# Optimization experiments

Measured on AMD Instinct MI355X. Metric: run time of the kernel, lower is better.

The kernel has to match this reference:

```python
import jax, jax.numpy as jnp
import numpy as np

B, S, INPUT_DIM = 16, 2048, 768
G, V = 2, 320            # num_codebooks, codebook_size
D = INPUT_DIM // G       # codebook_dim = 384
OUT_DIM = 768
TEMP = 1.0
EPS = 1e-10


def setup_inputs() -> dict:
    key = jax.random.key(0)
    ks = jax.random.split(key, 7)
    z = jax.random.normal(ks[0], (B, S, INPUT_DIM), dtype=jnp.float32)
    noise = jax.random.uniform(ks[1], (B, S, G, V), dtype=jnp.float32)
    # logits_projection: Linear(codebook_dim -> codebook_size)
    W_logits = jax.random.normal(ks[2], (D, V), dtype=jnp.float32) / np.sqrt(D)
    b_logits = jnp.zeros((V,), dtype=jnp.float32)
    codebooks = jax.random.normal(ks[3], (G, V, D), dtype=jnp.float32)
    # output_projection: Linear(input_dim -> output_dim)
    W_out = jax.random.normal(ks[4], (INPUT_DIM, OUT_DIM), dtype=jnp.float32) / np.sqrt(INPUT_DIM)
    b_out = jnp.zeros((OUT_DIM,), dtype=jnp.float32)
    return {"z": z, "noise": noise, "W_logits": W_logits, "b_logits": b_logits,
            "codebooks": codebooks, "W_out": W_out, "b_out": b_out}


def reference(z, noise, W_logits, b_logits, codebooks, W_out, b_out):
    b, s, _ = z.shape
    g, v, d = codebooks.shape
    zr = z.reshape(b, s, g, d)                                   # [B,S,G,D]
    logits = jnp.einsum('bsgd,dv->bsgv', zr, W_logits) + b_logits
    # training-mode gumbel noise
    gumbel = -jnp.log(-jnp.log(noise + EPS) + EPS)
    logits = (logits + gumbel) / TEMP
    probs = jax.nn.softmax(logits, axis=-1)                      # [B,S,G,V]
    indices = jnp.argmax(probs, axis=-1)                         # [B,S,G]
    hard = jax.nn.one_hot(indices, v, dtype=probs.dtype)
    quantized = hard - jax.lax.stop_gradient(probs) + probs      # straight-through
    quantized = jnp.einsum('bsgv,gvd->bsgd', quantized, codebooks)
    quantized = quantized.reshape(b, s, g * d)
    return quantized @ W_out + b_out
```

## Files before the change

kernel.cpp:

```cpp
#include <hip/hip_runtime.h>
#include <math.h>

#define BS_TOT 32768
#define IN_DIM 768
#define G_N 2
#define V_N 320
#define D_N 384
#define OUT_N 768
#define EPS_F 1e-10f

typedef _Float16 f16x8 __attribute__((ext_vector_type(8)));
typedef float    f32x16 __attribute__((ext_vector_type(16)));

#define GLOBAL_LOAD_LDS16(gaddr, laddr)                                        \
  __builtin_amdgcn_global_load_lds(                                            \
      (const __attribute__((address_space(1))) unsigned int*)(gaddr),          \
      (__attribute__((address_space(3))) unsigned int*)(laddr), 16, 0, 0)

__global__ __launch_bounds__(256) void prep_w(
    const float* __restrict__ Wl, _Float16* __restrict__ Wp)
{
    int e = blockIdx.x * 256 + threadIdx.x;
    if (e >= D_N * V_N) return;
    int k = e / V_N, v = e - k * V_N;
    int kt = k >> 5, kl = k & 31, kh = kl >> 3, j = kl & 7;
    float w = Wl[e];
    _Float16 a = (_Float16)w;
    float r = (w - (float)a) * 4096.f;
    Wp[((size_t)((kt * 2 + 0) * 4 + kh) * V_N + v) * 8 + j] = a;
    Wp[((size_t)((kt * 2 + 1) * 4 + kh) * V_N + v) * 8 + j] = (_Float16)r;
}

__global__ __launch_bounds__(256) void precompute_P(
    const float* __restrict__ cb, const float* __restrict__ Wo,
    float* __restrict__ P)
{
    const int tid = threadIdx.x;
    const int c0  = blockIdx.x * 256;
    const int r0  = blockIdx.y * 8;
    const int g   = r0 / V_N;
    __shared__ float As[8][D_N];
    {
        const float4* src = (const float4*)(cb + (size_t)r0 * D_N);
        float4* dst = (float4*)(&As[0][0]);
        #pragma unroll
        for (int p = 0; p < 3; ++p) dst[tid + p * 256] = src[tid + p * 256];
    }
    __syncthreads();
    float acc[8];
    #pragma unroll
    for (int i = 0; i < 8; ++i) acc[i] = 0.f;
    const float* wp = Wo + ((size_t)g * D_N) * OUT_N + c0 + tid;
    for (int d = 0; d < D_N; d += 4) {
        float w0 = wp[(size_t)(d + 0) * OUT_N];
        float w1 = wp[(size_t)(d + 1) * OUT_N];
        float w2 = wp[(size_t)(d + 2) * OUT_N];
        float w3 = wp[(size_t)(d + 3) * OUT_N];
        #pragma unroll
        for (int i = 0; i < 8; ++i) {
            float4 a = *(const float4*)&As[i][d];
            acc[i] = fmaf(a.x, w0, acc[i]);
            acc[i] = fmaf(a.y, w1, acc[i]);
            acc[i] = fmaf(a.z, w2, acc[i]);
            acc[i] = fmaf(a.w, w3, acc[i]);
        }
    }
    #pragma unroll
    for (int i = 0; i < 8; ++i)
        P[(size_t)(r0 + i) * OUT_N + c0 + tid] = acc[i];
}

__global__ __launch_bounds__(256, 2) void logits_mfma(
    const float* __restrict__ z, const float* __restrict__ noise,
    const f16x8* __restrict__ Wp, const float* __restrict__ bl,
    int* __restrict__ idx)
{
    const int tid  = threadIdx.x;
    const int g    = blockIdx.y;
    const int m0   = blockIdx.x * 64;
    const int ln   = tid & 63;
    const int wv   = tid >> 6;
    const int wrow = wv >> 1;
    const int wcol = wv & 1;
    const int lh   = ln >> 5;
    const int l5   = ln & 31;

    __shared__ f16x8 BsV[2560];
    __shared__ f16x8 AsV[512];
    __shared__ float sVal[2][64];
    __shared__ int   sIdx[2][64];

    f32x16 accM[5], accC[5];
    #pragma unroll
    for (int nf = 0; nf < 5; ++nf)
        #pragma unroll
        for (int i = 0; i < 16; ++i) { accM[nf][i] = 0.f; accC[nf][i] = 0.f; }

    const int arow_s = tid & 63;
    const int akh    = tid >> 6;
    const float* zrow = z + (size_t)(m0 + arow_s) * IN_DIM + g * D_N + akh * 8;

    float4 ap0 = *(const float4*)(zrow);
    float4 ap1 = *(const float4*)(zrow + 4);

    const int arow = wrow * 32 + l5;
    const int bcol = wcol * 160 + l5;

    for (int kt = 0; kt < 12; ++kt) {
        __syncthreads();
        #pragma unroll
        for (int p = 0; p < 10; ++p) {
            GLOBAL_LOAD_LDS16(Wp + (size_t)kt * 2560 + wv * 640 + p * 64 + ln,
                              BsV + wv * 640 + p * 64);
        }
        {
            float x[8] = {ap0.x, ap0.y, ap0.z, ap0.w, ap1.x, ap1.y, ap1.z, ap1.w};
            f16x8 h1, h2;
            #pragma unroll
            for (int i = 0; i < 8; ++i) {
                _Float16 a = (_Float16)x[i];
                float r = (x[i] - (float)a) * 4096.f;
                h1[i] = a;
                h2[i] = (_Float16)r;
            }
            AsV[(0 * 4 + akh) * 64 + arow_s] = h1;
            AsV[(1 * 4 + akh) * 64 + arow_s] = h2;
        }
        __syncthreads();
        if (kt < 11) {
            ap0 = *(const float4*)(zrow + (kt + 1) * 32);
            ap1 = *(const float4*)(zrow + (kt + 1) * 32 + 4);
        }
        #pragma unroll
        for (int b = 0; b < 2; ++b) {
            f16x8 a0 = AsV[(0 * 4 + b * 2 + lh) * 64 + arow];
            f16x8 a1 = AsV[(1 * 4 + b * 2 + lh) * 64 + arow];
            #pragma unroll
            for (int nf = 0; nf < 5; ++nf) {
                f16x8 b0 = BsV[(0 * 4 + b * 2 + lh) * 320 + bcol + nf * 32];
                f16x8 b1 = BsV[(1 * 4 + b * 2 + lh) * 320 + bcol + nf * 32];
                accM[nf] = __builtin_amdgcn_mfma_f32_32x32x16_f16(a0, b0, accM[nf], 0, 0, 0);
                accC[nf] = __builtin_amdgcn_mfma_f32_32x32x16_f16(a0, b1, accC[nf], 0, 0, 0);
                accC[nf] = __builtin_amdgcn_mfma_f32_32x32x16_f16(a1, b0, accC[nf], 0, 0, 0);
            }
        }
    }

    float blv[5];
    #pragma unroll
    for (int nf = 0; nf < 5; ++nf) blv[nf] = bl[wcol * 160 + nf * 32 + l5];

    #pragma unroll
    for (int r = 0; r < 16; ++r) {
        const int rowloc = (r & 3) + 8 * (r >> 2) + 4 * lh;
        const int grow   = m0 + wrow * 32 + rowloc;
        const float* np_ = noise + ((size_t)grow * G_N + g) * V_N + wcol * 160 + l5;
        float best = -INFINITY; int bi = 0;
        #pragma unroll
        for (int nf = 0; nf < 5; ++nf) {
            float u   = np_[nf * 32];
            float gum = -__logf(-__logf(u + EPS_F) + EPS_F);
            float v   = accM[nf][r] + 2.44140625e-4f * accC[nf][r] + blv[nf] + gum;
            int   c   = wcol * 160 + nf * 32 + l5;
            if (v > best) { best = v; bi = c; }
        }
        #pragma unroll
        for (int off = 1; off < 32; off <<= 1) {
            float ov = __shfl_xor(best, off);
            int   oi = __shfl_xor(bi, off);
            if (ov > best || (ov == best && oi < bi)) { best = ov; bi = oi; }
        }
        if (l5 == 0) {
            sVal[wcol][wrow * 32 + rowloc] = best;
            sIdx[wcol][wrow * 32 + rowloc] = bi;
        }
    }
    __syncthreads();
    if (tid < 64) {
        float v0 = sVal[0][tid], v1 = sVal[1][tid];
        int   i0 = sIdx[0][tid], i1 = sIdx[1][tid];
        int   b  = (v1 > v0 || (v1 == v0 && i1 < i0)) ? i1 : i0;
        idx[(size_t)(m0 + tid) * G_N + g] = b;
    }
}

__global__ __launch_bounds__(256) void gather_out(
    const float* __restrict__ P, const int* __restrict__ idx,
    const float* __restrict__ bo, float* __restrict__ out)
{
    const int tid  = threadIdx.x;
    const int row0 = blockIdx.x << 2;
    #pragma unroll
    for (int p = 0; p < 3; ++p) {
        int f   = tid + (p << 8);
        int rl  = f / 192;
        int c4  = f - rl * 192;
        int row = row0 + rl;
        int i0  = idx[row * 2];
        int i1  = idx[row * 2 + 1];
        float4 a  = ((const float4*)(P + (size_t)i0 * OUT_N))[c4];
        float4 b2 = ((const float4*)(P + (size_t)(V_N + i1) * OUT_N))[c4];
        float4 c  = ((const float4*)bo)[c4];
        float4 r;
        r.x = a.x + b2.x + c.x;
        r.y = a.y + b2.y + c.y;
        r.z = a.z + b2.z + c.z;
        r.w = a.w + b2.w + c.w;
        ((float4*)(out + (size_t)row * OUT_N))[c4] = r;
    }
}

extern "C" void kernel_launch(void* const* d_in, const int* in_sizes, int n_in,
                              void* d_out, int out_size, void* d_ws, size_t ws_size,
                              hipStream_t stream)
{
    const float* z     = (const float*)d_in[0];
    const float* noise = (const float*)d_in[1];
    const float* Wl    = (const float*)d_in[2];
    const float* bl    = (const float*)d_in[3];
    const float* cb    = (const float*)d_in[4];
    const float* Wo    = (const float*)d_in[5];
    const float* bo    = (const float*)d_in[6];
    float* out = (float*)d_out;

    float*     P   = (float*)d_ws;
    int*       idx = (int*)((char*)d_ws + 1966080);
    _Float16*  Wp  = (_Float16*)((char*)d_ws + 2228224);

    prep_w<<<(D_N * V_N + 255) / 256, 256, 0, stream>>>(Wl, Wp);

    dim3 gA(OUT_N / 256, (G_N * V_N) / 8);
    precompute_P<<<gA, 256, 0, stream>>>(cb, Wo, P);

    dim3 gB(BS_TOT / 64, G_N);
    logits_mfma<<<gB, 256, 0, stream>>>(z, noise, (const f16x8*)Wp, bl, idx);

    gather_out<<<BS_TOT / 4, 256, 0, stream>>>(P, idx, bo, out);
}
```

Measured before the change: 338.3 us.

## Fuse logits argmax with codebook gather and double-buffer K tiles

The logits kernel now handles both codebook groups inside one block and writes the output rows itself from the precomputed P table, which removes the separate gather kernel and the global idx round trip. The K loop is split into 16-wide steps with double-buffered LDS for the weight and activation tiles. Each iteration prefetches the next tile before its MFMAs and uses one barrier per step instead of two. The trade-offs are half as many blocks (512), more serial work per block, and only 128 threads producing the A tiles.

```diff
diff --git a/kernel.cpp b/kernel.cpp
--- a/kernel.cpp
+++ b/kernel.cpp
@@ -23,12 +23,12 @@
     int e = blockIdx.x * 256 + threadIdx.x;
     if (e >= D_N * V_N) return;
     int k = e / V_N, v = e - k * V_N;
-    int kt = k >> 5, kl = k & 31, kh = kl >> 3, j = kl & 7;
+    int t = k >> 4, kh = (k >> 3) & 1, j = k & 7;
     float w = Wl[e];
     _Float16 a = (_Float16)w;
     float r = (w - (float)a) * 4096.f;
-    Wp[((size_t)((kt * 2 + 0) * 4 + kh) * V_N + v) * 8 + j] = a;
-    Wp[((size_t)((kt * 2 + 1) * 4 + kh) * V_N + v) * 8 + j] = (_Float16)r;
+    Wp[((size_t)((t * 2 + 0) * 2 + kh) * V_N + v) * 8 + j] = a;
+    Wp[((size_t)((t * 2 + 1) * 2 + kh) * V_N + v) * 8 + j] = (_Float16)r;
 }
 
 __global__ __launch_bounds__(256) void precompute_P(
@@ -70,13 +70,13 @@
         P[(size_t)(r0 + i) * OUT_N + c0 + tid] = acc[i];
 }
 
-__global__ __launch_bounds__(256, 2) void logits_mfma(
+__global__ __launch_bounds__(256, 2) void logits_fused(
     const float* __restrict__ z, const float* __restrict__ noise,
     const f16x8* __restrict__ Wp, const float* __restrict__ bl,
-    int* __restrict__ idx)
+    const float* __restrict__ P, const float* __restrict__ bo,
+    float* __restrict__ out)
 {
     const int tid  = threadIdx.x;
-    const int g    = blockIdx.y;
     const int m0   = blockIdx.x * 64;
     const int ln   = tid & 63;
     const int wv   = tid >> 6;
@@ -85,36 +85,41 @@
     const int lh   = ln >> 5;
     const int l5   = ln & 31;
 
-    __shared__ f16x8 BsV[2560];
-    __shared__ f16x8 AsV[512];
+    __shared__ f16x8 BsV[2][1280];
+    __shared__ f16x8 AsV[2][256];
     __shared__ float sVal[2][64];
     __shared__ int   sIdx[2][64];
-
-    f32x16 accM[5], accC[5];
-    #pragma unroll
-    for (int nf = 0; nf < 5; ++nf)
-        #pragma unroll
-        for (int i = 0; i < 16; ++i) { accM[nf][i] = 0.f; accC[nf][i] = 0.f; }
-
-    const int arow_s = tid & 63;
-    const int akh    = tid >> 6;
-    const float* zrow = z + (size_t)(m0 + arow_s) * IN_DIM + g * D_N + akh * 8;
-
-    float4 ap0 = *(const float4*)(zrow);
-    float4 ap1 = *(const float4*)(zrow + 4);
+    __shared__ int   sFin[2][64];
 
     const int arow = wrow * 32 + l5;
     const int bcol = wcol * 160 + l5;
 
-    for (int kt = 0; kt < 12; ++kt) {
-        __syncthreads();
-        #pragma unroll
-        for (int p = 0; p < 10; ++p) {
-            GLOBAL_LOAD_LDS16(Wp + (size_t)kt * 2560 + wv * 640 + p * 64 + ln,
-                              BsV + wv * 640 + p * 64);
-        }
-        {
-            float x[8] = {ap0.x, ap0.y, ap0.z, ap0.w, ap1.x, ap1.y, ap1.z, ap1.w};
+    const int  prow  = tid & 63;
+    const int  pkh   = tid >> 6;
+    const bool aprod = (tid < 128);
+
+    float blv[5];
+    #pragma unroll
+    for (int nf = 0; nf < 5; ++nf) blv[nf] = bl[wcol * 160 + nf * 32 + l5];
+
+    for (int g = 0; g < 2; ++g) {
+        f32x16 accM[5], accC[5];
+        #pragma unroll
+        for (int nf = 0; nf < 5; ++nf)
+            #pragma unroll
+            for (int i = 0; i < 16; ++i) { accM[nf][i] = 0.f; accC[nf][i] = 0.f; }
+
+        const float* zb = z + (size_t)(m0 + prow) * IN_DIM + g * D_N + pkh * 8;
+        float4 az0 = {0.f, 0.f, 0.f, 0.f}, az1 = {0.f, 0.f, 0.f, 0.f};
+
+        #pragma unroll
+        for (int p = 0; p < 5; ++p)
+            GLOBAL_LOAD_LDS16(Wp + (wv * 5 + p) * 64 + ln,
+                              &BsV[0][(wv * 5 + p) * 64]);
+        if (aprod) {
+            float4 q0 = *(const float4*)(zb);
+            float4 q1 = *(const float4*)(zb + 4);
+            float x[8] = {q0.x, q0.y, q0.z, q0.w, q1.x, q1.y, q1.z, q1.w};
             f16x8 h1, h2;
             #pragma unroll
             for (int i = 0; i < 8; ++i) {
@@ -123,90 +128,107 @@
                 h1[i] = a;
                 h2[i] = (_Float16)r;
             }
-            AsV[(0 * 4 + akh) * 64 + arow_s] = h1;
-            AsV[(1 * 4 + akh) * 64 + arow_s] = h2;
+            AsV[0][(0 + pkh) * 64 + prow] = h1;
+            AsV[0][(2 + pkh) * 64 + prow] = h2;
+            az0 = *(const float4*)(zb + 16);
+            az1 = *(const float4*)(zb + 20);
         }
         __syncthreads();
-        if (kt < 11) {
-            ap0 = *(const float4*)(zrow + (kt + 1) * 32);
-            ap1 = *(const float4*)(zrow + (kt + 1) * 32 + 4);
-        }
-        #pragma unroll
-        for (int b = 0; b < 2; ++b) {
-            f16x8 a0 = AsV[(0 * 4 + b * 2 + lh) * 64 + arow];
-            f16x8 a1 = AsV[(1 * 4 + b * 2 + lh) * 64 + arow];
+
+        #pragma unroll 2
+        for (int t = 0; t < 24; ++t) {
+            const int cb  = t & 1;
+            const int nb  = cb ^ 1;
+            const int nxt = t + 1;
+            if (nxt < 24) {
+                #pragma unroll
+                for (int p = 0; p < 5; ++p)
+                    GLOBAL_LOAD_LDS16(Wp + (size_t)nxt * 1280 + (wv * 5 + p) * 64 + ln,
+                                      &BsV[nb][(wv * 5 + p) * 64]);
+                if (aprod) {
+                    float x[8] = {az0.x, az0.y, az0.z, az0.w,
+                                  az1.x, az1.y, az1.z, az1.w};
+                    f16x8 h1, h2;
+                    #pragma unroll
+                    for (int i = 0; i < 8; ++i) {
+                        _Float16 a = (_Float16)x[i];
+                        float r = (x[i] - (float)a) * 4096.f;
+                        h1[i] = a;
+                        h2[i] = (_Float16)r;
+                    }
+                    AsV[nb][(0 + pkh) * 64 + prow] = h1;
+                    AsV[nb][(2 + pkh) * 64 + prow] = h2;
+                    if (nxt + 1 < 24) {
+                        az0 = *(const float4*)(zb + (size_t)(nxt + 1) * 16);
+                        az1 = *(const float4*)(zb + (size_t)(nxt + 1) * 16 + 4);
+                    }
+                }
+            }
+            f16x8 A0 = AsV[cb][(0 + lh) * 64 + arow];
+            f16x8 A1 = AsV[cb][(2 + lh) * 64 + arow];
             #pragma unroll
             for (int nf = 0; nf < 5; ++nf) {
-                f16x8 b0 = BsV[(0 * 4 + b * 2 + lh) * 320 + bcol + nf * 32];
-                f16x8 b1 = BsV[(1 * 4 + b * 2 + lh) * 320 + bcol + nf * 32];
-                accM[nf] = __builtin_amdgcn_mfma_f32_32x32x16_f16(a0, b0, accM[nf], 0, 0, 0);
-                accC[nf] = __builtin_amdgcn_mfma_f32_32x32x16_f16(a0, b1, accC[nf], 0, 0, 0);
-                accC[nf] = __builtin_amdgcn_mfma_f32_32x32x16_f16(a1, b0, accC[nf], 0, 0, 0);
-            }
-        }
-    }
-
-    float blv[5];
-    #pragma unroll
-    for (int nf = 0; nf < 5; ++nf) blv[nf] = bl[wcol * 160 + nf * 32 + l5];
-
-    #pragma unroll
-    for (int r = 0; r < 16; ++r) {
-        const int rowloc = (r & 3) + 8 * (r >> 2) + 4 * lh;
-        const int grow   = m0 + wrow * 32 + rowloc;
-        const float* np_ = noise + ((size_t)grow * G_N + g) * V_N + wcol * 160 + l5;
-        float best = -INFINITY; int bi = 0;
-        #pragma unroll
-        for (int nf = 0; nf < 5; ++nf) {
-            float u   = np_[nf * 32];
-            float gum = -__logf(-__logf(u + EPS_F) + EPS_F);
-            float v   = accM[nf][r] + 2.44140625e-4f * accC[nf][r] + blv[nf] + gum;
-            int   c   = wcol * 160 + nf * 32 + l5;
-            if (v > best) { best = v; bi = c; }
-        }
-        #pragma unroll
-        for (int off = 1; off < 32; off <<= 1) {
-            float ov = __shfl_xor(best, off);
-            int   oi = __shfl_xor(bi, off);
-            if (ov > best || (ov == best && oi < bi)) { best = ov; bi = oi; }
-        }
-        if (l5 == 0) {
-            sVal[wcol][wrow * 32 + rowloc] = best;
-            sIdx[wcol][wrow * 32 + rowloc] = bi;
+                f16x8 B0 = BsV[cb][(0 + lh) * 320 + bcol + nf * 32];
+                f16x8 B1 = BsV[cb][(2 + lh) * 320 + bcol + nf * 32];
+                accM[nf] = __builtin_amdgcn_mfma_f32_32x32x16_f16(A0, B0, accM[nf], 0, 0, 0);
+                accC[nf] = __builtin_amdgcn_mfma_f32_32x32x16_f16(A0, B1, accC[nf], 0, 0, 0);
+                accC[nf] = __builtin_amdgcn_mfma_f32_32x32x16_f16(A1, B0, accC[nf], 0, 0, 0);
+            }
+            __syncthreads();
+        }
+
+        #pragma unroll
+        for (int r = 0; r < 16; ++r) {
+            const int rowloc = (r & 3) + 8 * (r >> 2) + 4 * lh;
+            const int grow   = m0 + wrow * 32 + rowloc;
+            const float* np_ = noise + ((size_t)grow * G_N + g) * V_N + wcol * 160 + l5;
+            float best = -INFINITY; int bi = 0;
+            #pragma unroll
+            for (int nf = 0; nf < 5; ++nf) {
+                float u   = np_[nf * 32];
+                float gum = -__logf(-__logf(u + EPS_F) + EPS_F);
+                float v   = accM[nf][r] + 2.44140625e-4f * accC[nf][r] + blv[nf] + gum;
+                int   c   = wcol * 160 + nf * 32 + l5;
+                if (v > best) { best = v; bi = c; }
+            }
+            #pragma unroll
+            for (int off = 1; off < 32; off <<= 1) {
+                float ov = __shfl_xor(best, off);
+                int   oi = __shfl_xor(bi, off);
+                if (ov > best || (ov == best && oi < bi)) { best = ov; bi = oi; }
+            }
+            if (l5 == 0) {
+                sVal[wcol][wrow * 32 + rowloc] = best;
+                sIdx[wcol][wrow * 32 + rowloc] = bi;
+            }
+        }
+        __syncthreads();
+        if (tid < 64) {
+            float v0 = sVal[0][tid], v1 = sVal[1][tid];
+            int   i0 = sIdx[0][tid], i1 = sIdx[1][tid];
+            sFin[g][tid] = (v1 > v0 || (v1 == v0 && i1 < i0)) ? i1 : i0;
         }
     }
     __syncthreads();
-    if (tid < 64) {
-        float v0 = sVal[0][tid], v1 = sVal[1][tid];
-        int   i0 = sIdx[0][tid], i1 = sIdx[1][tid];
-        int   b  = (v1 > v0 || (v1 == v0 && i1 < i0)) ? i1 : i0;
-        idx[(size_t)(m0 + tid) * G_N + g] = b;
-    }
-}
-
-__global__ __launch_bounds__(256) void gather_out(
-    const float* __restrict__ P, const int* __restrict__ idx,
-    const float* __restrict__ bo, float* __restrict__ out)
-{
-    const int tid  = threadIdx.x;
-    const int row0 = blockIdx.x << 2;
-    #pragma unroll
-    for (int p = 0; p < 3; ++p) {
-        int f   = tid + (p << 8);
-        int rl  = f / 192;
-        int c4  = f - rl * 192;
-        int row = row0 + rl;
-        int i0  = idx[row * 2];
-        int i1  = idx[row * 2 + 1];
-        float4 a  = ((const float4*)(P + (size_t)i0 * OUT_N))[c4];
-        float4 b2 = ((const float4*)(P + (size_t)(V_N + i1) * OUT_N))[c4];
-        float4 c  = ((const float4*)bo)[c4];
+
+    const float4* Pv  = (const float4*)P;
+    const float4* bov = (const float4*)bo;
+    #pragma unroll 4
+    for (int p = 0; p < 48; ++p) {
+        int f  = p * 256 + tid;
+        int rl = f / 192;
+        int c4 = f - rl * 192;
+        int i0 = sFin[0][rl];
+        int i1 = sFin[1][rl];
+        float4 a  = Pv[(size_t)i0 * 192 + c4];
+        float4 b2 = Pv[(size_t)(V_N + i1) * 192 + c4];
+        float4 c  = bov[c4];
         float4 r;
         r.x = a.x + b2.x + c.x;
         r.y = a.y + b2.y + c.y;
         r.z = a.z + b2.z + c.z;
         r.w = a.w + b2.w + c.w;
-        ((float4*)(out + (size_t)row * OUT_N))[c4] = r;
+        ((float4*)(out + (size_t)(m0 + rl) * OUT_N))[c4] = r;
     }
 }
 
@@ -223,17 +245,14 @@
     const float* bo    = (const float*)d_in[6];
     float* out = (float*)d_out;
 
-    float*     P   = (float*)d_ws;
-    int*       idx = (int*)((char*)d_ws + 1966080);
-    _Float16*  Wp  = (_Float16*)((char*)d_ws + 2228224);
+    float*     P  = (float*)d_ws;
+    _Float16*  Wp = (_Float16*)((char*)d_ws + 1966080);
 
     prep_w<<<(D_N * V_N + 255) / 256, 256, 0, stream>>>(Wl, Wp);
 
     dim3 gA(OUT_N / 256, (G_N * V_N) / 8);
     precompute_P<<<gA, 256, 0, stream>>>(cb, Wo, P);
 
-    dim3 gB(BS_TOT / 64, G_N);
-    logits_mfma<<<gB, 256, 0, stream>>>(z, noise, (const f16x8*)Wp, bl, idx);
-
-    gather_out<<<BS_TOT / 4, 256, 0, stream>>>(P, idx, bo, out);
-}
+    logits_fused<<<BS_TOT / 64, 256, 0, stream>>>(
+        z, noise, (const f16x8*)Wp, bl, P, bo, out);
+}
```

New measurement: 347.0 us. +2.6%, slower.

## Split logits GEMM over vocab chunks with resident weights and partial argmax

Applied to the files above, without the earlier changes.

The logits kernel now gives each block a 64-column slice of the codebook vocabulary. The whole K-extent of the split-f16 weight slice stays resident in LDS, loaded once, so the per-K-tile weight reloads and barriers disappear. Each block covers 256 rows and software-pipelines its z loads three steps ahead in registers. Each block writes a partial max and index per row, and the gather kernel reduces the five partials before indexing the precomputed codebook-projection table. In exchange, z is re-read five times per codebook, partial results add an extra global round trip, and occupancy is lowered to one block per CU.

```diff
diff --git a/kernel.cpp b/kernel.cpp
--- a/kernel.cpp
+++ b/kernel.cpp
@@ -23,12 +23,15 @@
     int e = blockIdx.x * 256 + threadIdx.x;
     if (e >= D_N * V_N) return;
     int k = e / V_N, v = e - k * V_N;
-    int kt = k >> 5, kl = k & 31, kh = kl >> 3, j = kl & 7;
+    int c = v >> 6, col = v & 63;
+    int t = k >> 4, kh = (k >> 3) & 1, j = k & 7;
     float w = Wl[e];
     _Float16 a = (_Float16)w;
     float r = (w - (float)a) * 4096.f;
-    Wp[((size_t)((kt * 2 + 0) * 4 + kh) * V_N + v) * 8 + j] = a;
-    Wp[((size_t)((kt * 2 + 1) * 4 + kh) * V_N + v) * 8 + j] = (_Float16)r;
+    size_t u0 = (size_t)c * 6144 + ((t * 2 + 0) * 2 + kh) * 64 + col;
+    size_t u1 = (size_t)c * 6144 + ((t * 2 + 1) * 2 + kh) * 64 + col;
+    Wp[u0 * 8 + j] = a;
+    Wp[u1 * 8 + j] = (_Float16)r;
 }
 
 __global__ __launch_bounds__(256) void precompute_P(
@@ -70,51 +73,57 @@
         P[(size_t)(r0 + i) * OUT_N + c0 + tid] = acc[i];
 }
 
-__global__ __launch_bounds__(256, 2) void logits_mfma(
+__global__ __launch_bounds__(256, 1) void logits_part(
     const float* __restrict__ z, const float* __restrict__ noise,
     const f16x8* __restrict__ Wp, const float* __restrict__ bl,
-    int* __restrict__ idx)
-{
-    const int tid  = threadIdx.x;
-    const int g    = blockIdx.y;
-    const int m0   = blockIdx.x * 64;
-    const int ln   = tid & 63;
-    const int wv   = tid >> 6;
-    const int wrow = wv >> 1;
-    const int wcol = wv & 1;
-    const int lh   = ln >> 5;
-    const int l5   = ln & 31;
-
-    __shared__ f16x8 BsV[2560];
-    __shared__ f16x8 AsV[512];
-    __shared__ float sVal[2][64];
-    __shared__ int   sIdx[2][64];
-
-    f32x16 accM[5], accC[5];
-    #pragma unroll
-    for (int nf = 0; nf < 5; ++nf)
-        #pragma unroll
-        for (int i = 0; i < 16; ++i) { accM[nf][i] = 0.f; accC[nf][i] = 0.f; }
-
-    const int arow_s = tid & 63;
-    const int akh    = tid >> 6;
-    const float* zrow = z + (size_t)(m0 + arow_s) * IN_DIM + g * D_N + akh * 8;
-
-    float4 ap0 = *(const float4*)(zrow);
-    float4 ap1 = *(const float4*)(zrow + 4);
-
-    const int arow = wrow * 32 + l5;
-    const int bcol = wcol * 160 + l5;
-
-    for (int kt = 0; kt < 12; ++kt) {
-        __syncthreads();
-        #pragma unroll
-        for (int p = 0; p < 10; ++p) {
-            GLOBAL_LOAD_LDS16(Wp + (size_t)kt * 2560 + wv * 640 + p * 64 + ln,
-                              BsV + wv * 640 + p * 64);
-        }
-        {
-            float x[8] = {ap0.x, ap0.y, ap0.z, ap0.w, ap1.x, ap1.y, ap1.z, ap1.w};
+    float* __restrict__ pv, int* __restrict__ pi)
+{
+    const int tid = threadIdx.x;
+    const int ln  = tid & 63;
+    const int wv  = tid >> 6;
+    const int lh  = ln >> 5;
+    const int l5  = ln & 31;
+    const int cg  = blockIdx.x;
+    const int cc  = cg % 5;
+    const int g   = cg / 5;
+    const int m0  = blockIdx.y * 256;
+
+    __shared__ f16x8 Bs[6144];
+
+    const f16x8* wsrc = Wp + (size_t)cc * 6144;
+    #pragma unroll
+    for (int r2 = 0; r2 < 24; ++r2)
+        GLOBAL_LOAD_LDS16(wsrc + r2 * 256 + wv * 64 + ln, Bs + r2 * 256 + wv * 64);
+
+    const float* zb = z + (size_t)(m0 + wv * 64 + l5) * IN_DIM + g * D_N + lh * 8;
+    float4 bufA[4], bufB[4], bufC[4];
+    #pragma unroll
+    for (int q = 0; q < 2; ++q) {
+        const float* zq = zb + (size_t)q * 32 * IN_DIM;
+        bufA[q * 2]     = *(const float4*)(zq + 0);
+        bufA[q * 2 + 1] = *(const float4*)(zq + 4);
+        bufB[q * 2]     = *(const float4*)(zq + 16);
+        bufB[q * 2 + 1] = *(const float4*)(zq + 20);
+        bufC[q * 2]     = *(const float4*)(zq + 32);
+        bufC[q * 2 + 1] = *(const float4*)(zq + 36);
+    }
+
+    f32x16 aM[2][2], aC[2][2];
+    #pragma unroll
+    for (int q = 0; q < 2; ++q)
+        #pragma unroll
+        for (int nf = 0; nf < 2; ++nf)
+            #pragma unroll
+            for (int i = 0; i < 16; ++i) { aM[q][nf][i] = 0.f; aC[q][nf][i] = 0.f; }
+
+    __syncthreads();
+
+    auto step = [&](float4 (&buf)[4], int t) {
+        f16x8 A0[2], A1[2];
+        #pragma unroll
+        for (int q = 0; q < 2; ++q) {
+            float x[8] = {buf[q * 2].x, buf[q * 2].y, buf[q * 2].z, buf[q * 2].w,
+                          buf[q * 2 + 1].x, buf[q * 2 + 1].y, buf[q * 2 + 1].z, buf[q * 2 + 1].w};
             f16x8 h1, h2;
             #pragma unroll
             for (int i = 0; i < 8; ++i) {
@@ -123,90 +132,111 @@
                 h1[i] = a;
                 h2[i] = (_Float16)r;
             }
-            AsV[(0 * 4 + akh) * 64 + arow_s] = h1;
-            AsV[(1 * 4 + akh) * 64 + arow_s] = h2;
-        }
-        __syncthreads();
-        if (kt < 11) {
-            ap0 = *(const float4*)(zrow + (kt + 1) * 32);
-            ap1 = *(const float4*)(zrow + (kt + 1) * 32 + 4);
-        }
-        #pragma unroll
-        for (int b = 0; b < 2; ++b) {
-            f16x8 a0 = AsV[(0 * 4 + b * 2 + lh) * 64 + arow];
-            f16x8 a1 = AsV[(1 * 4 + b * 2 + lh) * 64 + arow];
-            #pragma unroll
-            for (int nf = 0; nf < 5; ++nf) {
-                f16x8 b0 = BsV[(0 * 4 + b * 2 + lh) * 320 + bcol + nf * 32];
-                f16x8 b1 = BsV[(1 * 4 + b * 2 + lh) * 320 + bcol + nf * 32];
-                accM[nf] = __builtin_amdgcn_mfma_f32_32x32x16_f16(a0, b0, accM[nf], 0, 0, 0);
-                accC[nf] = __builtin_amdgcn_mfma_f32_32x32x16_f16(a0, b1, accC[nf], 0, 0, 0);
-                accC[nf] = __builtin_amdgcn_mfma_f32_32x32x16_f16(a1, b0, accC[nf], 0, 0, 0);
-            }
-        }
-    }
-
-    float blv[5];
-    #pragma unroll
-    for (int nf = 0; nf < 5; ++nf) blv[nf] = bl[wcol * 160 + nf * 32 + l5];
-
-    #pragma unroll
-    for (int r = 0; r < 16; ++r) {
-        const int rowloc = (r & 3) + 8 * (r >> 2) + 4 * lh;
-        const int grow   = m0 + wrow * 32 + rowloc;
-        const float* np_ = noise + ((size_t)grow * G_N + g) * V_N + wcol * 160 + l5;
-        float best = -INFINITY; int bi = 0;
-        #pragma unroll
-        for (int nf = 0; nf < 5; ++nf) {
-            float u   = np_[nf * 32];
-            float gum = -__logf(-__logf(u + EPS_F) + EPS_F);
-            float v   = accM[nf][r] + 2.44140625e-4f * accC[nf][r] + blv[nf] + gum;
-            int   c   = wcol * 160 + nf * 32 + l5;
-            if (v > best) { best = v; bi = c; }
-        }
-        #pragma unroll
-        for (int off = 1; off < 32; off <<= 1) {
-            float ov = __shfl_xor(best, off);
-            int   oi = __shfl_xor(bi, off);
-            if (ov > best || (ov == best && oi < bi)) { best = ov; bi = oi; }
-        }
-        if (l5 == 0) {
-            sVal[wcol][wrow * 32 + rowloc] = best;
-            sIdx[wcol][wrow * 32 + rowloc] = bi;
-        }
-    }
-    __syncthreads();
-    if (tid < 64) {
-        float v0 = sVal[0][tid], v1 = sVal[1][tid];
-        int   i0 = sIdx[0][tid], i1 = sIdx[1][tid];
-        int   b  = (v1 > v0 || (v1 == v0 && i1 < i0)) ? i1 : i0;
-        idx[(size_t)(m0 + tid) * G_N + g] = b;
-    }
-}
-
-__global__ __launch_bounds__(256) void gather_out(
-    const float* __restrict__ P, const int* __restrict__ idx,
-    const float* __restrict__ bo, float* __restrict__ out)
+            A0[q] = h1; A1[q] = h2;
+        }
+        if (t + 3 < 24) {
+            #pragma unroll
+            for (int q = 0; q < 2; ++q) {
+                const float* zq = zb + (size_t)q * 32 * IN_DIM + (t + 3) * 16;
+                buf[q * 2]     = *(const float4*)(zq);
+                buf[q * 2 + 1] = *(const float4*)(zq + 4);
+            }
+        }
+        #pragma unroll
+        for (int nf = 0; nf < 2; ++nf) {
+            f16x8 B0 = Bs[((t * 2 + 0) * 2 + lh) * 64 + nf * 32 + l5];
+            f16x8 B1 = Bs[((t * 2 + 1) * 2 + lh) * 64 + nf * 32 + l5];
+            #pragma unroll
+            for (int q = 0; q < 2; ++q) {
+                aM[q][nf] = __builtin_amdgcn_mfma_f32_32x32x16_f16(A0[q], B0, aM[q][nf], 0, 0, 0);
+                aC[q][nf] = __builtin_amdgcn_mfma_f32_32x32x16_f16(A0[q], B1, aC[q][nf], 0, 0, 0);
+                aC[q][nf] = __builtin_amdgcn_mfma_f32_32x32x16_f16(A1[q], B0, aC[q][nf], 0, 0, 0);
+            }
+        }
+    };
+    #pragma unroll
+    for (int tt = 0; tt < 24; tt += 3) {
+        step(bufA, tt);
+        step(bufB, tt + 1);
+        step(bufC, tt + 2);
+    }
+
+    float blv[2];
+    #pragma unroll
+    for (int nf = 0; nf < 2; ++nf) blv[nf] = bl[cc * 64 + nf * 32 + l5];
+
+    #pragma unroll
+    for (int q = 0; q < 2; ++q) {
+        #pragma unroll
+        for (int r = 0; r < 16; ++r) {
+            const int rowloc = (r & 3) + 8 * (r >> 2) + 4 * lh;
+            const int grow   = m0 + wv * 64 + q * 32 + rowloc;
+            const float* np_ = noise + ((size_t)grow * G_N + g) * V_N + cc * 64 + l5;
+            float best = -INFINITY; int bi = 0;
+            #pragma unroll
+            for (int nf = 0; nf < 2; ++nf) {
+                float u   = np_[nf * 32];
+                float gum = -__logf(-__logf(u + EPS_F) + EPS_F);
+                float v   = aM[q][nf][r] + 2.44140625e-4f * aC[q][nf][r] + blv[nf] + gum;
+                int   c   = cc * 64 + nf * 32 + l5;
+                if (v > best) { best = v; bi = c; }
+            }
+            #pragma unroll
+            for (int off = 1; off < 32; off <<= 1) {
+                float ov = __shfl_xor(best, off);
+                int   oi = __shfl_xor(bi, off);
+                if (ov > best || (ov == best && oi < bi)) { best = ov; bi = oi; }
+            }
+            if (l5 == 0) {
+                pv[(size_t)(g * 5 + cc) * BS_TOT + grow] = best;
+                pi[(size_t)(g * 5 + cc) * BS_TOT + grow] = bi;
+            }
+        }
+    }
+}
+
+__global__ __launch_bounds__(256) void finish_gather(
+    const float* __restrict__ P, const float* __restrict__ pv,
+    const int* __restrict__ pi, const float* __restrict__ bo,
+    float* __restrict__ out)
 {
     const int tid  = threadIdx.x;
     const int row0 = blockIdx.x << 2;
+    __shared__ int sI[2][4];
+    if (tid < 8) {
+        const int gg  = tid >> 2, rl = tid & 3;
+        const int row = row0 + rl;
+        const float* pvb = pv + (size_t)gg * 5 * BS_TOT + row;
+        const int*   pib = pi + (size_t)gg * 5 * BS_TOT + row;
+        float best = pvb[0];
+        int   bi   = pib[0];
+        #pragma unroll
+        for (int c = 1; c < 5; ++c) {
+            float v = pvb[(size_t)c * BS_TOT];
+            int   i = pib[(size_t)c * BS_TOT];
+            if (v > best) { best = v; bi = i; }
+        }
+        sI[gg][rl] = bi;
+    }
+    __syncthreads();
+    const float4* Pv  = (const float4*)P;
+    const float4* bov = (const float4*)bo;
     #pragma unroll
     for (int p = 0; p < 3; ++p) {
         int f   = tid + (p << 8);
         int rl  = f / 192;
         int c4  = f - rl * 192;
-        int row = row0 + rl;
-        int i0  = idx[row * 2];
-        int i1  = idx[row * 2 + 1];
-        float4 a  = ((const float4*)(P + (size_t)i0 * OUT_N))[c4];
-        float4 b2 = ((const float4*)(P + (size_t)(V_N + i1) * OUT_N))[c4];
-        float4 c  = ((const float4*)bo)[c4];
+        int i0  = sI[0][rl];
+        int i1  = sI[1][rl];
+        float4 a  = Pv[(size_t)i0 * 192 + c4];
+        float4 b2 = Pv[(size_t)(V_N + i1) * 192 + c4];
+        float4 c  = bov[c4];
         float4 r;
         r.x = a.x + b2.x + c.x;
         r.y = a.y + b2.y + c.y;
         r.z = a.z + b2.z + c.z;
         r.w = a.w + b2.w + c.w;
-        ((float4*)(out + (size_t)row * OUT_N))[c4] = r;
+        ((float4*)(out + (size_t)(row0 + rl) * OUT_N))[c4] = r;
     }
 }
 
@@ -223,17 +253,18 @@
     const float* bo    = (const float*)d_in[6];
     float* out = (float*)d_out;
 
-    float*     P   = (float*)d_ws;
-    int*       idx = (int*)((char*)d_ws + 1966080);
-    _Float16*  Wp  = (_Float16*)((char*)d_ws + 2228224);
+    float*     P  = (float*)d_ws;
+    float*     pv = (float*)((char*)d_ws + 1966080);
+    int*       pi = (int*)((char*)d_ws + 3276800);
+    _Float16*  Wp = (_Float16*)((char*)d_ws + 4587520);
 
     prep_w<<<(D_N * V_N + 255) / 256, 256, 0, stream>>>(Wl, Wp);
 
     dim3 gA(OUT_N / 256, (G_N * V_N) / 8);
     precompute_P<<<gA, 256, 0, stream>>>(cb, Wo, P);
 
-    dim3 gB(BS_TOT / 64, G_N);
-    logits_mfma<<<gB, 256, 0, stream>>>(z, noise, (const f16x8*)Wp, bl, idx);
-
-    gather_out<<<BS_TOT / 4, 256, 0, stream>>>(P, idx, bo, out);
-}
+    dim3 gB(10, BS_TOT / 256);
+    logits_part<<<gB, 256, 0, stream>>>(z, noise, (const f16x8*)Wp, bl, pv, pi);
+
+    finish_gather<<<BS_TOT / 4, 256, 0, stream>>>(P, pv, pi, bo, out);
+}
```

New measurement: 496.9 us. 46.9% more time.
